# Kernel optimization log

Hardware: AMD Instinct MI355X
Metric: run time of the kernel (lower is better)

Reference implementation:

```python
import jax, jax.numpy as jnp
import numpy as np

N = 50000      # num_nodes
E = 400000     # num_edges
ND = 128       # node_dim (== hidden_dim of GraphNetwork)
HID = 128      # per-head hidden dim in GAT layer
HEADS = 4      # GAT default num_heads
L = 3          # num_layers


def setup_inputs() -> dict:
    key = jax.random.key(0)
    ks = jax.random.split(key, 12)
    s = lambda k, shape, fan: (jax.random.normal(k, shape, jnp.float32) / np.sqrt(fan)).astype(jnp.float32)
    return dict(
        node_features=jax.random.normal(ks[0], (N, ND), jnp.float32),
        edge_index=jax.random.randint(ks[1], (2, E), 0, N, dtype=jnp.int32),
        enc_w1=s(ks[2], (ND, HID), ND), enc_b1=jnp.zeros((HID,), jnp.float32),
        enc_w2=s(ks[3], (HID, HID), HID), enc_b2=jnp.zeros((HID,), jnp.float32),
        gat_W=s(ks[4], (L, HID, HEADS * HID), HID),
        gat_a_src=s(ks[5], (L, HEADS, HID), HID),
        gat_a_dst=s(ks[6], (L, HEADS, HID), HID),
        gat_out_w=s(ks[7], (L, HEADS * HID, HID), HEADS * HID),
        gat_out_b=jnp.zeros((L, HID), jnp.float32),
        out_w1=s(ks[8], (HID, HID), HID), out_b1=jnp.zeros((HID,), jnp.float32),
        out_w2=s(ks[9], (HID, HID), HID), out_b2=jnp.zeros((HID,), jnp.float32),
    )


def _gat_layer(x, row, col, W, a_src, a_dst, ow, ob):
    """One GraphAttentionLayer (eval mode: dropout disabled)."""
    n = x.shape[0]
    h = (x @ W).reshape(n, HEADS, HID)                       # [N,H,D]
    # per-node attention logits (equivalent to (h[row]*a_src).sum(-1) gathered)
    s_src = jnp.einsum('nhd,hd->nh', h, a_src)               # [N,H]
    s_dst = jnp.einsum('nhd,hd->nh', h, a_dst)               # [N,H]
    e = s_src[row] + s_dst[col]                              # [E,H]
    e = jnp.where(e > 0, e, 0.2 * e)                         # LeakyReLU(0.2)
    e_exp = jnp.exp(e)                                       # matches torch: raw exp, no max-shift
    e_sum = jax.ops.segment_sum(e_exp, col, num_segments=n)  # [N,H]
    alpha = e_exp / (e_sum[col] + 1e-8)                      # [E,H]
    msg = h[row] * alpha[:, :, None]                         # [E,H,D]
    out = jax.ops.segment_sum(msg, col, num_segments=n)      # [N,H,D]
    out = out.reshape(n, HEADS * HID) @ ow + ob              # out_proj
    return x + out                                           # residual


def reference(node_features, edge_index, enc_w1, enc_b1, enc_w2, enc_b2,
              gat_W, gat_a_src, gat_a_dst, gat_out_w, gat_out_b,
              out_w1, out_b1, out_w2, out_b2):
    row, col = edge_index[0], edge_index[1]
    # node encoder: Linear-ReLU-Linear
    h = jax.nn.relu(node_features @ enc_w1 + enc_b1) @ enc_w2 + enc_b2
    for i in range(L):
        h = _gat_layer(h, row, col, gat_W[i], gat_a_src[i], gat_a_dst[i],
                       gat_out_w[i], gat_out_b[i])
    # output MLP: Linear-ReLU-Linear
    h = jax.nn.relu(h @ out_w1 + out_b1) @ out_w2 + out_b2
    # batch is None, global_pooling='mean'
    graph_embedding = h.mean(axis=0, keepdims=True)          # [1,HID]
    return h, graph_embedding
```

## Files before the change

kernel.cpp:

```cpp
#include <hip/hip_runtime.h>
#include <math.h>

typedef unsigned short ushort_t;
typedef __attribute__((ext_vector_type(8))) unsigned short ushortx8;
typedef __attribute__((ext_vector_type(4))) unsigned short ushortx4;
typedef __attribute__((ext_vector_type(4))) float floatx4;
typedef __attribute__((ext_vector_type(8))) short frag8;

__device__ __forceinline__ float bf2f(ushort_t u){
  union {unsigned int i; float f;} v; v.i = ((unsigned int)u)<<16; return v.f;
}
__device__ __forceinline__ ushort_t f2bf(float f){
  union {float f; unsigned int i;} v; v.f = f;
  unsigned int x = v.i;
  unsigned int r = x + 0x7fffu + ((x>>16)&1u);
  return (ushort_t)(r>>16);
}

__device__ __forceinline__ void gload16(const void* g, void* l){
  __builtin_amdgcn_global_load_lds(
      (const __attribute__((address_space(1))) unsigned int*)g,
      (__attribute__((address_space(3))) unsigned int*)l, 16, 0, 0);
}

__global__ __launch_bounds__(256) void k_count(const int* __restrict__ col, int* __restrict__ cnt, int E){
  int e = blockIdx.x*256 + threadIdx.x;
  if (e < E) atomicAdd(&cnt[col[e]], 1);
}

__global__ __launch_bounds__(256) void k_scan1(const int* __restrict__ cnt, int* __restrict__ offs,
                                               int* __restrict__ partials, int n){
  __shared__ int buf[256];
  int tid = threadIdx.x;
  int gid = blockIdx.x*256 + tid;
  int v = (gid < n) ? cnt[gid] : 0;
  buf[tid] = v; __syncthreads();
  #pragma unroll
  for (int off=1; off<256; off<<=1){
    int t = (tid >= off) ? buf[tid-off] : 0;
    __syncthreads();
    buf[tid] += t;
    __syncthreads();
  }
  if (gid < n) offs[gid] = buf[tid] - v;
  if (tid == 255) partials[blockIdx.x] = buf[255];
}

__global__ __launch_bounds__(256) void k_scan2(int* __restrict__ partials, int nb){
  __shared__ int buf[256];
  int tid = threadIdx.x;
  int v = (tid < nb) ? partials[tid] : 0;
  buf[tid] = v; __syncthreads();
  #pragma unroll
  for (int off=1; off<256; off<<=1){
    int t = (tid >= off) ? buf[tid-off] : 0;
    __syncthreads();
    buf[tid] += t;
    __syncthreads();
  }
  partials[tid] = buf[tid] - v;
}

__global__ __launch_bounds__(256) void k_scan3(int* __restrict__ offs, const int* __restrict__ partials,
                                               int n, int E){
  int gid = blockIdx.x*256 + threadIdx.x;
  if (gid < n) offs[gid] += partials[blockIdx.x];
  if (blockIdx.x == 0 && threadIdx.x == 0) offs[n] = E;
}

__global__ __launch_bounds__(256) void k_fill(const int* __restrict__ row, const int* __restrict__ col,
                                              const int* __restrict__ offs, int* __restrict__ fill,
                                              int* __restrict__ rowS, int E){
  int e = blockIdx.x*256 + threadIdx.x;
  if (e >= E) return;
  int c = col[e];
  int pos = offs[c] + atomicAdd(&fill[c], 1);
  rowS[pos] = row[e];
}

template<int K, int NC, int CNT>
__global__ __launch_bounds__(256) void k_convT_b(const float* __restrict__ src, ushort_t* __restrict__ dst){
  int idx = blockIdx.x*256 + threadIdx.x;
  if (idx >= CNT*K*NC) return;
  int l = idx / (K*NC);
  int rem = idx - l*(K*NC);
  int k = rem / NC, n = rem - k*NC;
  dst[(size_t)l*K*NC + (size_t)n*K + k] = f2bf(src[idx]);
}

__global__ __launch_bounds__(256) void k_convT4(const float* __restrict__ s0, const float* __restrict__ s1,
                                                const float* __restrict__ s2, const float* __restrict__ s3,
                                                ushort_t* __restrict__ d0, ushort_t* __restrict__ d1,
                                                ushort_t* __restrict__ d2, ushort_t* __restrict__ d3){
  int idx = blockIdx.x*256 + threadIdx.x;
  if (idx >= 4*16384) return;
  int which = idx >> 14;
  int rem = idx & 16383;
  int k = rem >> 7, n = rem & 127;
  const float* s = which==0 ? s0 : which==1 ? s1 : which==2 ? s2 : s3;
  ushort_t*    d = which==0 ? d0 : which==1 ? d1 : which==2 ? d2 : d3;
  d[n*128 + k] = f2bf(s[rem]);
}


__device__ __forceinline__ void la_store(ushort_t* LA, int row, int col, ushort_t v){
  LA[row*128 + ((((col>>3) ^ (row&7))<<3) | (col&7))] = v;
}
__device__ __forceinline__ void la_store8(ushort_t* LA, int row, int cg, ushortx8 v){
  *(ushortx8*)&LA[row*128 + ((cg ^ (row&7))<<3)] = v;
}

__device__ __forceinline__ void stage_tile128_swz(const ushort_t* src, int ld, int row0, int M, int kc,
                                                  ushort_t* lds, int tid){
  #pragma unroll
  for (int i=0;i<8;i++){
    int chunk = tid + 256*i;
    int r = chunk>>4, cg = chunk&15;
    int gr = row0 + r; if (gr >= M) gr = M-1;
    int scg = cg ^ (r&7);
    gload16(src + (size_t)gr*ld + kc + scg*8, (char*)lds + (size_t)chunk*16);
  }
}

template<int NKS>
__device__ __forceinline__ void gemm_swzA_gB(const ushort_t* LA, const ushort_t* __restrict__ BT, int ldb,
                                             floatx4 (&acc)[4][4], int wr,int wc,int lm,int lk){
  #pragma unroll
  for (int ks=0; ks<NKS; ks++){
    frag8 b[4];
    #pragma unroll
    for (int ni=0;ni<4;ni++)
      b[ni] = *(const frag8*)&BT[(size_t)(wc+ni*16+lm)*ldb + ks*32 + lk];
    frag8 a[4];
    int cg = ks*4 + (lk>>3);
    #pragma unroll
    for (int mi=0;mi<4;mi++){
      int row = wr + mi*16 + lm;
      a[mi] = *(const frag8*)&LA[row*128 + ((cg ^ (row&7))<<3)];
    }
    #pragma unroll
    for (int mi=0;mi<4;mi++)
      #pragma unroll
      for (int ni=0;ni<4;ni++)
        acc[mi][ni] = __builtin_amdgcn_mfma_f32_16x16x32_bf16(a[mi], b[ni], acc[mi][ni], 0, 0, 0);
  }
}

__device__ __forceinline__ void zero_acc(floatx4 (&acc)[4][4]){
  #pragma unroll
  for (int i=0;i<4;i++)
    #pragma unroll
    for (int j=0;j<4;j++) acc[i][j] = floatx4{0.f,0.f,0.f,0.f};
}

__device__ __forceinline__ void sdst_block(const floatx4 (&acc)[4][4],
    const float* avec_s, const float* avec_d, float* s_src, float* s_dst, float* sred,
    int head, int bm, int M, int tid, int wid, int lane, int wr, int wc, int lm, int lr4){
  float avs[4], avd[4];
  #pragma unroll
  for (int ni=0;ni<4;ni++){
    int d = wc + ni*16 + lm;
    avs[ni] = avec_s[head*128 + d];
    avd[ni] = avec_d[head*128 + d];
  }
  float pss[4][4], psd[4][4];
  #pragma unroll
  for (int mi=0;mi<4;mi++){
    #pragma unroll
    for (int r=0;r<4;r++){
      float vs = 0.f, vd = 0.f;
      #pragma unroll
      for (int ni=0;ni<4;ni++){
        float v = acc[mi][ni][r];
        vs += v * avs[ni];
        vd += v * avd[ni];
      }
      #pragma unroll
      for (int m=1;m<16;m<<=1){
        vs += __shfl_xor(vs, m);
        vd += __shfl_xor(vd, m);
      }
      pss[mi][r] = vs; psd[mi][r] = vd;
    }
  }
  if (lm == 0){
    #pragma unroll
    for (int mi=0;mi<4;mi++)
      #pragma unroll
      for (int r=0;r<4;r++){
        int rl = wr + mi*16 + lr4 + r;
        sred[0*256 + (wid&1)*128 + rl] = pss[mi][r];
        sred[1*256 + (wid&1)*128 + rl] = psd[mi][r];
      }
  }
  __syncthreads();
  int sd = tid >> 7, rl = tid & 127;
  float v = sred[sd*256 + rl] + sred[sd*256 + 128 + rl];
  int rowg = bm + rl;
  if (rowg < M) (sd ? s_dst : s_src)[(size_t)rowg*4 + head] = v;
}

__device__ __forceinline__ void wgemm_heads(const ushort_t* LA,
    const ushort_t* __restrict__ WT, const float* avs, const float* avd,
    ushort_t* h, float* s_src, float* s_dst, float* sred,
    int bm, int M, int tid, int wid, int lane, int wr, int wc, int lm, int lk, int lr4){
  for (int hb=0; hb<4; hb++){
    __syncthreads();
    floatx4 acc[4][4]; zero_acc(acc);
    gemm_swzA_gB<4>(LA, WT + (size_t)hb*16384, 128, acc, wr, wc, lm, lk);
    #pragma unroll
    for (int mi=0;mi<4;mi++){
      #pragma unroll
      for (int ni=0;ni<4;ni++){
        int colg = wc + ni*16 + lm;
        #pragma unroll
        for (int r=0;r<4;r++){
          int rowg = bm + wr + mi*16 + lr4 + r;
          if (rowg < M) h[(size_t)rowg*512 + hb*128 + colg] = f2bf(acc[mi][ni][r]);
        }
      }
    }
    sdst_block(acc, avs, avd, s_src, s_dst, sred, hb, bm, M, tid, wid, lane, wr, wc, lm, lr4);
  }
}

__global__ __launch_bounds__(256,3) void k_enc(
    const float* __restrict__ nodef,
    const ushort_t* __restrict__ e1T, const float* __restrict__ eb1,
    const ushort_t* __restrict__ e2T, const float* __restrict__ eb2,
    const ushort_t* __restrict__ WT, const float* __restrict__ avs, const float* __restrict__ avd,
    float* __restrict__ x, ushort_t* __restrict__ h,
    float* __restrict__ s_src, float* __restrict__ s_dst, int M)
{
  __shared__ ushort_t LA[128*128];
  __shared__ float sred[512];
  const int tid = threadIdx.x, wid = tid>>6, lane = tid&63;
  const int bm = blockIdx.x*128;
  const int wr = (wid>>1)*64, wc = (wid&1)*64, lm = lane&15, lk = (lane>>4)*8, lr4 = (lane>>4)*4;

  #pragma unroll
  for (int i=0;i<8;i++){
    int chunk = tid + 256*i;
    int r = chunk>>4, cg = chunk&15;
    int gr = bm + r; if (gr >= M) gr = M-1;
    floatx4 lo = *(const floatx4*)(nodef + (size_t)gr*128 + cg*8);
    floatx4 hi = *(const floatx4*)(nodef + (size_t)gr*128 + cg*8 + 4);
    ushortx8 v;
    #pragma unroll
    for (int j=0;j<4;j++){ v[j] = f2bf(lo[j]); v[j+4] = f2bf(hi[j]); }
    la_store8(LA, r, cg, v);
  }
  __syncthreads();

  floatx4 acc[4][4]; zero_acc(acc);
  gemm_swzA_gB<4>(LA, e1T, 128, acc, wr, wc, lm, lk);
  __syncthreads();
  #pragma unroll
  for (int mi=0;mi<4;mi++)
    #pragma unroll
    for (int ni=0;ni<4;ni++){
      int cl = wc + ni*16 + lm;
      float b = eb1[cl];
      #pragma unroll
      for (int r=0;r<4;r++){
        float v = acc[mi][ni][r] + b;
        v = v > 0.f ? v : 0.f;
        la_store(LA, wr + mi*16 + lr4 + r, cl, f2bf(v));
      }
    }
  __syncthreads();

  zero_acc(acc);
  gemm_swzA_gB<4>(LA, e2T, 128, acc, wr, wc, lm, lk);
  __syncthreads();
  #pragma unroll
  for (int mi=0;mi<4;mi++)
    #pragma unroll
    for (int ni=0;ni<4;ni++){
      int cl = wc + ni*16 + lm;
      float b = eb2[cl];
      #pragma unroll
      for (int r=0;r<4;r++){
        int rl = wr + mi*16 + lr4 + r;
        int rowg = bm + rl;
        float v = acc[mi][ni][r] + b;
        if (rowg < M) x[(size_t)rowg*128 + cl] = v;
        la_store(LA, rl, cl, f2bf(v));
      }
    }

  wgemm_heads(LA, WT, avs, avd, h, s_src, s_dst, sred,
              bm, M, tid, wid, lane, wr, wc, lm, lk, lr4);
}

__global__ __launch_bounds__(256,3) void k_mid(
    const ushort_t* __restrict__ msg, const ushort_t* __restrict__ OT, const float* __restrict__ ob,
    const ushort_t* __restrict__ WT, const float* __restrict__ avs, const float* __restrict__ avd,
    float* __restrict__ x, ushort_t* __restrict__ h,
    float* __restrict__ s_src, float* __restrict__ s_dst, int M)
{
  __shared__ ushort_t LA[128*128];
  __shared__ float sred[512];
  const int tid = threadIdx.x, wid = tid>>6, lane = tid&63;
  const int bm = blockIdx.x*128;
  const int wr = (wid>>1)*64, wc = (wid&1)*64, lm = lane&15, lk = (lane>>4)*8, lr4 = (lane>>4)*4;

  floatx4 acc[4][4]; zero_acc(acc);
  for (int kc = 0; kc < 512; kc += 128){
    stage_tile128_swz(msg, 512, bm, M, kc, LA, tid);
    __syncthreads();
    gemm_swzA_gB<4>(LA, OT + kc, 512, acc, wr, wc, lm, lk);
    __syncthreads();
  }
  #pragma unroll
  for (int mi=0;mi<4;mi++)
    #pragma unroll
    for (int ni=0;ni<4;ni++){
      int cl = wc + ni*16 + lm;
      float b = ob[cl];
      #pragma unroll
      for (int r=0;r<4;r++){
        int rl = wr + mi*16 + lr4 + r;
        int rowg = bm + rl;
        float v = acc[mi][ni][r] + b;
        if (rowg < M){
          v += x[(size_t)rowg*128 + cl];
          x[(size_t)rowg*128 + cl] = v;
        }
        la_store(LA, rl, cl, f2bf(v));
      }
    }

  wgemm_heads(LA, WT, avs, avd, h, s_src, s_dst, sred,
              bm, M, tid, wid, lane, wr, wc, lm, lk, lr4);
}

__global__ __launch_bounds__(256,3) void k_tail(
    const ushort_t* __restrict__ msg, const ushort_t* __restrict__ OT, const float* __restrict__ ob,
    const ushort_t* __restrict__ m1T, const float* __restrict__ mb1,
    const ushort_t* __restrict__ m2T, const float* __restrict__ mb2,
    const float* __restrict__ x, float* __restrict__ out, float* __restrict__ cpart, int M)
{
  __shared__ ushort_t LA[128*128];
  __shared__ float sredc[256];
  const int tid = threadIdx.x, wid = tid>>6, lane = tid&63;
  const int bm = blockIdx.x*128;
  const int wr = (wid>>1)*64, wc = (wid&1)*64, lm = lane&15, lk = (lane>>4)*8, lr4 = (lane>>4)*4;

  floatx4 acc[4][4]; zero_acc(acc);
  for (int kc = 0; kc < 512; kc += 128){
    stage_tile128_swz(msg, 512, bm, M, kc, LA, tid);
    __syncthreads();
    gemm_swzA_gB<4>(LA, OT + kc, 512, acc, wr, wc, lm, lk);
    __syncthreads();
  }
  #pragma unroll
  for (int mi=0;mi<4;mi++)
    #pragma unroll
    for (int ni=0;ni<4;ni++){
      int cl = wc + ni*16 + lm;
      float b = ob[cl];
      #pragma unroll
      for (int r=0;r<4;r++){
        int rl = wr + mi*16 + lr4 + r;
        int rowg = bm + rl;
        float v = acc[mi][ni][r] + b;
        if (rowg < M) v += x[(size_t)rowg*128 + cl];
        la_store(LA, rl, cl, f2bf(v));
      }
    }
  __syncthreads();

  zero_acc(acc);
  gemm_swzA_gB<4>(LA, m1T, 128, acc, wr, wc, lm, lk);
  __syncthreads();
  #pragma unroll
  for (int mi=0;mi<4;mi++)
    #pragma unroll
    for (int ni=0;ni<4;ni++){
      int cl = wc + ni*16 + lm;
      float b = mb1[cl];
      #pragma unroll
      for (int r=0;r<4;r++){
        float v = acc[mi][ni][r] + b;
        v = v > 0.f ? v : 0.f;
        la_store(LA, wr + mi*16 + lr4 + r, cl, f2bf(v));
      }
    }
  __syncthreads();

  zero_acc(acc);
  gemm_swzA_gB<4>(LA, m2T, 128, acc, wr, wc, lm, lk);

  float csum[4];
  #pragma unroll
  for (int i=0;i<4;i++) csum[i] = 0.f;
  #pragma unroll
  for (int mi=0;mi<4;mi++)
    #pragma unroll
    for (int ni=0;ni<4;ni++){
      int cl = wc + ni*16 + lm;
      float b = mb2[cl];
      #pragma unroll
      for (int r=0;r<4;r++){
        int rowg = bm + wr + mi*16 + lr4 + r;
        if (rowg < M){
          float v = acc[mi][ni][r] + b;
          out[(size_t)rowg*128 + cl] = v;
          csum[ni] += v;
        }
      }
    }
  __syncthreads();
  #pragma unroll
  for (int ni=0;ni<4;ni++){
    float cs = csum[ni];
    cs += __shfl_xor(cs, 16);
    cs += __shfl_xor(cs, 32);
    if (lane < 16) sredc[(wid>>1)*128 + wc + ni*16 + lane] = cs;
  }
  __syncthreads();
  if (tid < 128) cpart[(size_t)blockIdx.x*128 + tid] = sredc[tid] + sredc[128 + tid];
}

__global__ __launch_bounds__(256) void k_gather(const ushort_t* __restrict__ h,
    const float* __restrict__ s_src, const float* __restrict__ s_dst,
    const int* __restrict__ offs, const int* __restrict__ rowS,
    ushort_t* __restrict__ msg, int N)
{
  int wid = threadIdx.x >> 6, lane = threadIdx.x & 63;
  int n = blockIdx.x*4 + wid;
  if (n >= N) return;
  int beg = offs[n], end = offs[n+1];
  const int sub  = lane & 15;
  const int head = lane >> 4;
  const float sdv = s_dst[(size_t)n*4 + head];
  const int c0 = lane*8;

  float acc[8];
  #pragma unroll
  for (int k=0;k<8;k++) acc[k] = 0.f;
  float dsum = 0.f;

  for (int chunk = beg; chunk < end; chunk += 16){
    int m = end - chunk; if (m > 16) m = 16;
    int q = chunk + (sub < m ? sub : m-1);
    int r_p = rowS[q];
    float ss = s_src[(size_t)r_p*4 + head];
    float e = ss + sdv;
    e = e > 0.f ? e : 0.2f*e;
    float w = __expf(e);
    if (sub >= m) w = 0.f;
    dsum += w;

    int j = 0;
    for (; j+1 < m; j += 2){
      int r0 = __shfl(r_p, j);
      int r1 = __shfl(r_p, j+1);
      float w0 = __shfl(w, head*16 + j);
      float w1 = __shfl(w, head*16 + j+1);
      ushortx8 h0 = *(const ushortx8*)(h + (size_t)r0*512 + c0);
      ushortx8 h1 = *(const ushortx8*)(h + (size_t)r1*512 + c0);
      #pragma unroll
      for (int k=0;k<8;k++) acc[k] += w0 * bf2f(h0[k]);
      #pragma unroll
      for (int k=0;k<8;k++) acc[k] += w1 * bf2f(h1[k]);
    }
    if (j < m){
      int r0 = __shfl(r_p, j);
      float w0 = __shfl(w, head*16 + j);
      ushortx8 h0 = *(const ushortx8*)(h + (size_t)r0*512 + c0);
      #pragma unroll
      for (int k=0;k<8;k++) acc[k] += w0 * bf2f(h0[k]);
    }
  }

  float d = dsum;
  #pragma unroll
  for (int mask=1; mask<16; mask<<=1) d += __shfl_xor(d, mask);
  float invd = 1.0f / (d + 1e-8f);

  ushortx8 o;
  #pragma unroll
  for (int k=0;k<8;k++) o[k] = f2bf(acc[k]*invd);
  __builtin_nontemporal_store(o, (ushortx8*)(msg + (size_t)n*512 + c0));
}

__global__ __launch_bounds__(256) void k_csum2(const float* __restrict__ part, float* __restrict__ out,
                                               int nb, int N){
  __shared__ float buf[256];
  int c = threadIdx.x & 127, half = threadIdx.x >> 7;
  float s = 0.f;
  for (int b = half; b < nb; b += 2) s += part[(size_t)b*128 + c];
  buf[threadIdx.x] = s; __syncthreads();
  if (threadIdx.x < 128) out[c] = (buf[c] + buf[128 + c]) / (float)N;
}

extern "C" void kernel_launch(void* const* d_in, const int* in_sizes, int n_in,
                              void* d_out, int out_size, void* d_ws, size_t ws_size,
                              hipStream_t stream)
{
  const int N = in_sizes[0] / 128;
  const int E = in_sizes[1] / 2;

  const float* nodef  = (const float*)d_in[0];
  const int*   row    = (const int*)d_in[1];
  const int*   col    = row + E;
  const float* enc_w1 = (const float*)d_in[2];
  const float* enc_b1 = (const float*)d_in[3];
  const float* enc_w2 = (const float*)d_in[4];
  const float* enc_b2 = (const float*)d_in[5];
  const float* gat_W  = (const float*)d_in[6];
  const float* a_src  = (const float*)d_in[7];
  const float* a_dst  = (const float*)d_in[8];
  const float* out_w  = (const float*)d_in[9];
  const float* out_b  = (const float*)d_in[10];
  const float* w1     = (const float*)d_in[11];
  const float* b1     = (const float*)d_in[12];
  const float* w2     = (const float*)d_in[13];
  const float* b2     = (const float*)d_in[14];

  char* p = (char*)d_ws;
  auto alloc = [&](size_t bytes)->char*{
    char* r = p; p += (bytes + 255) & ~(size_t)255; return r;
  };
  float*    x     = (float*)   alloc((size_t)N*128*4);
  ushort_t* msg   = (ushort_t*)alloc((size_t)N*512*2);
  ushort_t* h     = (ushort_t*)alloc((size_t)N*512*2);
  float*    s_src = (float*)   alloc((size_t)N*4*4);
  float*    s_dst = (float*)   alloc((size_t)N*4*4);
  int*      offs  = (int*)     alloc(((size_t)N+1)*4);
  int*      rowS  = (int*)     alloc((size_t)E*4);
  int*      cnt   = (int*)     alloc((size_t)N*4);
  int*      fill  = (int*)     alloc((size_t)N*4);
  int*      parts = (int*)     alloc(1024);
  float*    cpart = (float*)   alloc((size_t)((N+127)/128)*128*4);
  ushort_t* wt_e1 = (ushort_t*)alloc(16384*2);
  ushort_t* wt_e2 = (ushort_t*)alloc(16384*2);
  ushort_t* wt_W  = (ushort_t*)alloc((size_t)3*65536*2);
  ushort_t* wt_o  = (ushort_t*)alloc((size_t)3*65536*2);
  ushort_t* wt_m1 = (ushort_t*)alloc(16384*2);
  ushort_t* wt_m2 = (ushort_t*)alloc(16384*2);

  hipMemsetAsync(cnt, 0, (size_t)N*4, stream);
  hipMemsetAsync(fill, 0, (size_t)N*4, stream);

  const int gE = (E + 255)/256;
  const int gN = (N + 255)/256;
  const int gW = (N + 3)/4;
  const int gy = (N + 127)/128;
  dim3 blk(256);

  k_count<<<gE, blk, 0, stream>>>(col, cnt, E);
  k_scan1<<<gN, blk, 0, stream>>>(cnt, offs, parts, N);
  k_scan2<<<1,  blk, 0, stream>>>(parts, gN);
  k_scan3<<<gN, blk, 0, stream>>>(offs, parts, N, E);
  k_fill <<<gE, blk, 0, stream>>>(row, col, offs, fill, rowS, E);

  k_convT4<<<(4*16384+255)/256, blk, 0, stream>>>(enc_w1, enc_w2, w1, w2, wt_e1, wt_e2, wt_m1, wt_m2);
  k_convT_b<128,512,3><<<(3*65536+255)/256, blk, 0, stream>>>(gat_W, wt_W);
  k_convT_b<512,128,3><<<(3*65536+255)/256, blk, 0, stream>>>(out_w, wt_o);

  k_enc<<<gy, blk, 0, stream>>>(nodef, wt_e1, enc_b1, wt_e2, enc_b2,
                                wt_W, a_src, a_dst, x, h, s_src, s_dst, N);

  for (int l = 0; l < 3; l++){
    k_gather<<<gW, blk, 0, stream>>>(h, s_src, s_dst, offs, rowS, msg, N);
    if (l < 2){
      k_mid<<<gy, blk, 0, stream>>>(msg, wt_o + (size_t)l*65536, out_b + (size_t)l*128,
                                    wt_W + (size_t)(l+1)*65536,
                                    a_src + (size_t)(l+1)*512, a_dst + (size_t)(l+1)*512,
                                    x, h, s_src, s_dst, N);
    } else {
      k_tail<<<gy, blk, 0, stream>>>(msg, wt_o + (size_t)2*65536, out_b + (size_t)2*128,
                                     wt_m1, b1, wt_m2, b2,
                                     x, (float*)d_out, cpart, N);
    }
  }
  k_csum2<<<1, blk, 0, stream>>>(cpart, (float*)d_out + (size_t)N*128, gy, N);
}
```

Before: 567.4 us.

## Split head GEMM across grid.y, stage B weights in LDS, ping-pong residual buffers

After: 670.1 us. 1.18x slower.

```diff
diff --git a/kernel.cpp b/kernel.cpp
--- a/kernel.cpp
+++ b/kernel.cpp
@@ -3,7 +3,6 @@
 
 typedef unsigned short ushort_t;
 typedef __attribute__((ext_vector_type(8))) unsigned short ushortx8;
-typedef __attribute__((ext_vector_type(4))) unsigned short ushortx4;
 typedef __attribute__((ext_vector_type(4))) float floatx4;
 typedef __attribute__((ext_vector_type(8))) short frag8;
 
@@ -110,33 +109,35 @@
   *(ushortx8*)&LA[row*128 + ((cg ^ (row&7))<<3)] = v;
 }
 
-__device__ __forceinline__ void stage_tile128_swz(const ushort_t* src, int ld, int row0, int M, int kc,
-                                                  ushort_t* lds, int tid){
-  #pragma unroll
-  for (int i=0;i<8;i++){
+__device__ __forceinline__ void stage64_swz(const ushort_t* __restrict__ src, int ld, int row0, int M,
+                                            int kc, ushort_t* lds, int tid){
+  #pragma unroll
+  for (int i=0;i<4;i++){
     int chunk = tid + 256*i;
-    int r = chunk>>4, cg = chunk&15;
+    int r = chunk>>3, cg = chunk&7;
     int gr = row0 + r; if (gr >= M) gr = M-1;
     int scg = cg ^ (r&7);
     gload16(src + (size_t)gr*ld + kc + scg*8, (char*)lds + (size_t)chunk*16);
   }
 }
 
-template<int NKS>
-__device__ __forceinline__ void gemm_swzA_gB(const ushort_t* LA, const ushort_t* __restrict__ BT, int ldb,
-                                             floatx4 (&acc)[4][4], int wr,int wc,int lm,int lk){
-  #pragma unroll
-  for (int ks=0; ks<NKS; ks++){
-    frag8 b[4];
-    #pragma unroll
-    for (int ni=0;ni<4;ni++)
-      b[ni] = *(const frag8*)&BT[(size_t)(wc+ni*16+lm)*ldb + ks*32 + lk];
-    frag8 a[4];
-    int cg = ks*4 + (lk>>3);
+template<int CWA>
+__device__ __forceinline__ void ldsgemm64(const ushort_t* LA, int kaoff, const ushort_t* LB,
+                                          floatx4 (&acc)[4][4], int wr,int wc,int lm,int lk){
+  #pragma unroll
+  for (int ks=0; ks<2; ks++){
+    frag8 a[4], b[4];
+    int cga = (kaoff + ks*32 + lk) >> 3;
     #pragma unroll
     for (int mi=0;mi<4;mi++){
       int row = wr + mi*16 + lm;
-      a[mi] = *(const frag8*)&LA[row*128 + ((cg ^ (row&7))<<3)];
+      a[mi] = *(const frag8*)&LA[row*(CWA*8) + ((cga ^ (row&7))<<3)];
+    }
+    int cgb = (ks*32 + lk) >> 3;
+    #pragma unroll
+    for (int ni=0;ni<4;ni++){
+      int row = wc + ni*16 + lm;
+      b[ni] = *(const frag8*)&LB[row*64 + ((cgb ^ (row&7))<<3)];
     }
     #pragma unroll
     for (int mi=0;mi<4;mi++)
@@ -153,63 +154,22 @@
     for (int j=0;j<4;j++) acc[i][j] = floatx4{0.f,0.f,0.f,0.f};
 }
 
-__device__ __forceinline__ void sdst_block(const floatx4 (&acc)[4][4],
-    const float* avec_s, const float* avec_d, float* s_src, float* s_dst, float* sred,
-    int head, int bm, int M, int tid, int wid, int lane, int wr, int wc, int lm, int lr4){
-  float avs[4], avd[4];
-  #pragma unroll
-  for (int ni=0;ni<4;ni++){
-    int d = wc + ni*16 + lm;
-    avs[ni] = avec_s[head*128 + d];
-    avd[ni] = avec_d[head*128 + d];
-  }
-  float pss[4][4], psd[4][4];
-  #pragma unroll
-  for (int mi=0;mi<4;mi++){
-    #pragma unroll
-    for (int r=0;r<4;r++){
-      float vs = 0.f, vd = 0.f;
-      #pragma unroll
-      for (int ni=0;ni<4;ni++){
-        float v = acc[mi][ni][r];
-        vs += v * avs[ni];
-        vd += v * avd[ni];
-      }
-      #pragma unroll
-      for (int m=1;m<16;m<<=1){
-        vs += __shfl_xor(vs, m);
-        vd += __shfl_xor(vd, m);
-      }
-      pss[mi][r] = vs; psd[mi][r] = vd;
-    }
-  }
-  if (lm == 0){
+__device__ __forceinline__ void wgemm_2heads(const ushort_t* LA, ushort_t* LB,
+    const ushort_t* __restrict__ WT, const float* __restrict__ avec_s, const float* __restrict__ avec_d,
+    ushort_t* __restrict__ h, float* __restrict__ s_src, float* __restrict__ s_dst, float* sred,
+    int by, int bm, int M, int tid, int wid, int lane, int wr, int wc, int lm, int lk, int lr4){
+  for (int hh=0; hh<2; hh++){
+    int hb = by*2 + hh;
+    floatx4 acc[4][4]; zero_acc(acc);
+    #pragma unroll
+    for (int kph=0; kph<2; kph++){
+      stage64_swz(WT + (size_t)hb*16384, 128, 0, 128, kph*64, LB, tid);
+      __syncthreads();
+      ldsgemm64<16>(LA, kph*64, LB, acc, wr, wc, lm, lk);
+      __syncthreads();
+    }
     #pragma unroll
     for (int mi=0;mi<4;mi++)
-      #pragma unroll
-      for (int r=0;r<4;r++){
-        int rl = wr + mi*16 + lr4 + r;
-        sred[0*256 + (wid&1)*128 + rl] = pss[mi][r];
-        sred[1*256 + (wid&1)*128 + rl] = psd[mi][r];
-      }
-  }
-  __syncthreads();
-  int sd = tid >> 7, rl = tid & 127;
-  float v = sred[sd*256 + rl] + sred[sd*256 + 128 + rl];
-  int rowg = bm + rl;
-  if (rowg < M) (sd ? s_dst : s_src)[(size_t)rowg*4 + head] = v;
-}
-
-__device__ __forceinline__ void wgemm_heads(const ushort_t* LA,
-    const ushort_t* __restrict__ WT, const float* avs, const float* avd,
-    ushort_t* h, float* s_src, float* s_dst, float* sred,
-    int bm, int M, int tid, int wid, int lane, int wr, int wc, int lm, int lk, int lr4){
-  for (int hb=0; hb<4; hb++){
-    __syncthreads();
-    floatx4 acc[4][4]; zero_acc(acc);
-    gemm_swzA_gB<4>(LA, WT + (size_t)hb*16384, 128, acc, wr, wc, lm, lk);
-    #pragma unroll
-    for (int mi=0;mi<4;mi++){
       #pragma unroll
       for (int ni=0;ni<4;ni++){
         int colg = wc + ni*16 + lm;
@@ -219,8 +179,44 @@
           if (rowg < M) h[(size_t)rowg*512 + hb*128 + colg] = f2bf(acc[mi][ni][r]);
         }
       }
-    }
-    sdst_block(acc, avs, avd, s_src, s_dst, sred, hb, bm, M, tid, wid, lane, wr, wc, lm, lr4);
+    float avs[4], avd[4];
+    #pragma unroll
+    for (int ni=0;ni<4;ni++){
+      int d = wc + ni*16 + lm;
+      avs[ni] = avec_s[hb*128 + d];
+      avd[ni] = avec_d[hb*128 + d];
+    }
+    #pragma unroll
+    for (int mi=0;mi<4;mi++){
+      #pragma unroll
+      for (int r=0;r<4;r++){
+        float vs = 0.f, vd = 0.f;
+        #pragma unroll
+        for (int ni=0;ni<4;ni++){
+          float v = acc[mi][ni][r];
+          vs += v * avs[ni];
+          vd += v * avd[ni];
+        }
+        #pragma unroll
+        for (int m=1;m<16;m<<=1){
+          vs += __shfl_xor(vs, m);
+          vd += __shfl_xor(vd, m);
+        }
+        if (lm == 0){
+          int rl = wr + mi*16 + lr4 + r;
+          int half = wid & 1;
+          sred[((hh*2+0)*2 + half)*128 + rl] = vs;
+          sred[((hh*2+1)*2 + half)*128 + rl] = vd;
+        }
+      }
+    }
+  }
+  __syncthreads();
+  for (int q = tid; q < 512; q += 256){
+    int hh = q >> 8, sd = (q >> 7) & 1, rl = q & 127;
+    float v = sred[((hh*2+sd)*2+0)*128 + rl] + sred[((hh*2+sd)*2+1)*128 + rl];
+    int rowg = bm + rl;
+    if (rowg < M) (sd ? s_dst : s_src)[(size_t)rowg*4 + by*2 + hh] = v;
   }
 }
 
@@ -229,13 +225,14 @@
     const ushort_t* __restrict__ e1T, const float* __restrict__ eb1,
     const ushort_t* __restrict__ e2T, const float* __restrict__ eb2,
     const ushort_t* __restrict__ WT, const float* __restrict__ avs, const float* __restrict__ avd,
-    float* __restrict__ x, ushort_t* __restrict__ h,
+    float* __restrict__ xout, ushort_t* __restrict__ h,
     float* __restrict__ s_src, float* __restrict__ s_dst, int M)
 {
   __shared__ ushort_t LA[128*128];
-  __shared__ float sred[512];
+  __shared__ ushort_t LB[128*64];
+  __shared__ float sred[1024];
   const int tid = threadIdx.x, wid = tid>>6, lane = tid&63;
-  const int bm = blockIdx.x*128;
+  const int bm = blockIdx.x*128, by = blockIdx.y;
   const int wr = (wid>>1)*64, wc = (wid&1)*64, lm = lane&15, lk = (lane>>4)*8, lr4 = (lane>>4)*4;
 
   #pragma unroll
@@ -253,8 +250,13 @@
   __syncthreads();
 
   floatx4 acc[4][4]; zero_acc(acc);
-  gemm_swzA_gB<4>(LA, e1T, 128, acc, wr, wc, lm, lk);
-  __syncthreads();
+  #pragma unroll
+  for (int kph=0; kph<2; kph++){
+    stage64_swz(e1T, 128, 0, 128, kph*64, LB, tid);
+    __syncthreads();
+    ldsgemm64<16>(LA, kph*64, LB, acc, wr, wc, lm, lk);
+    __syncthreads();
+  }
   #pragma unroll
   for (int mi=0;mi<4;mi++)
     #pragma unroll
@@ -268,11 +270,14 @@
         la_store(LA, wr + mi*16 + lr4 + r, cl, f2bf(v));
       }
     }
-  __syncthreads();
-
   zero_acc(acc);
-  gemm_swzA_gB<4>(LA, e2T, 128, acc, wr, wc, lm, lk);
-  __syncthreads();
+  #pragma unroll
+  for (int kph=0; kph<2; kph++){
+    stage64_swz(e2T, 128, 0, 128, kph*64, LB, tid);
+    __syncthreads();
+    ldsgemm64<16>(LA, kph*64, LB, acc, wr, wc, lm, lk);
+    __syncthreads();
+  }
   #pragma unroll
   for (int mi=0;mi<4;mi++)
     #pragma unroll
@@ -284,32 +289,34 @@
         int rl = wr + mi*16 + lr4 + r;
         int rowg = bm + rl;
         float v = acc[mi][ni][r] + b;
-        if (rowg < M) x[(size_t)rowg*128 + cl] = v;
+        if (by == 0 && rowg < M) xout[(size_t)rowg*128 + cl] = v;
         la_store(LA, rl, cl, f2bf(v));
       }
     }
 
-  wgemm_heads(LA, WT, avs, avd, h, s_src, s_dst, sred,
-              bm, M, tid, wid, lane, wr, wc, lm, lk, lr4);
+  wgemm_2heads(LA, LB, WT, avs, avd, h, s_src, s_dst, sred,
+               by, bm, M, tid, wid, lane, wr, wc, lm, lk, lr4);
 }
 
 __global__ __launch_bounds__(256,3) void k_mid(
     const ushort_t* __restrict__ msg, const ushort_t* __restrict__ OT, const float* __restrict__ ob,
     const ushort_t* __restrict__ WT, const float* __restrict__ avs, const float* __restrict__ avd,
-    float* __restrict__ x, ushort_t* __restrict__ h,
+    const float* __restrict__ xin, float* __restrict__ xout, ushort_t* __restrict__ h,
     float* __restrict__ s_src, float* __restrict__ s_dst, int M)
 {
   __shared__ ushort_t LA[128*128];
-  __shared__ float sred[512];
+  __shared__ ushort_t LB[128*64];
+  __shared__ float sred[1024];
   const int tid = threadIdx.x, wid = tid>>6, lane = tid&63;
-  const int bm = blockIdx.x*128;
+  const int bm = blockIdx.x*128, by = blockIdx.y;
   const int wr = (wid>>1)*64, wc = (wid&1)*64, lm = lane&15, lk = (lane>>4)*8, lr4 = (lane>>4)*4;
 
   floatx4 acc[4][4]; zero_acc(acc);
-  for (int kc = 0; kc < 512; kc += 128){
-    stage_tile128_swz(msg, 512, bm, M, kc, LA, tid);
-    __syncthreads();
-    gemm_swzA_gB<4>(LA, OT + kc, 512, acc, wr, wc, lm, lk);
+  for (int kc = 0; kc < 512; kc += 64){
+    stage64_swz(msg, 512, bm, M, kc, LA, tid);
+    stage64_swz(OT,  512, 0, 128, kc, LB, tid);
+    __syncthreads();
+    ldsgemm64<8>(LA, 0, LB, acc, wr, wc, lm, lk);
     __syncthreads();
   }
   #pragma unroll
@@ -324,34 +331,36 @@
         int rowg = bm + rl;
         float v = acc[mi][ni][r] + b;
         if (rowg < M){
-          v += x[(size_t)rowg*128 + cl];
-          x[(size_t)rowg*128 + cl] = v;
+          v += xin[(size_t)rowg*128 + cl];
+          if (by == 0) xout[(size_t)rowg*128 + cl] = v;
         }
         la_store(LA, rl, cl, f2bf(v));
       }
     }
 
-  wgemm_heads(LA, WT, avs, avd, h, s_src, s_dst, sred,
-              bm, M, tid, wid, lane, wr, wc, lm, lk, lr4);
+  wgemm_2heads(LA, LB, WT, avs, avd, h, s_src, s_dst, sred,
+               by, bm, M, tid, wid, lane, wr, wc, lm, lk, lr4);
 }
 
 __global__ __launch_bounds__(256,3) void k_tail(
     const ushort_t* __restrict__ msg, const ushort_t* __restrict__ OT, const float* __restrict__ ob,
     const ushort_t* __restrict__ m1T, const float* __restrict__ mb1,
     const ushort_t* __restrict__ m2T, const float* __restrict__ mb2,
-    const float* __restrict__ x, float* __restrict__ out, float* __restrict__ cpart, int M)
+    const float* __restrict__ xin, float* __restrict__ out, float* __restrict__ cpart, int M)
 {
   __shared__ ushort_t LA[128*128];
-  __shared__ float sredc[256];
+  __shared__ ushort_t LB[128*64];
+  __shared__ float sred[1024];
   const int tid = threadIdx.x, wid = tid>>6, lane = tid&63;
   const int bm = blockIdx.x*128;
   const int wr = (wid>>1)*64, wc = (wid&1)*64, lm = lane&15, lk = (lane>>4)*8, lr4 = (lane>>4)*4;
 
   floatx4 acc[4][4]; zero_acc(acc);
-  for (int kc = 0; kc < 512; kc += 128){
-    stage_tile128_swz(msg, 512, bm, M, kc, LA, tid);
-    __syncthreads();
-    gemm_swzA_gB<4>(LA, OT + kc, 512, acc, wr, wc, lm, lk);
+  for (int kc = 0; kc < 512; kc += 64){
+    stage64_swz(msg, 512, bm, M, kc, LA, tid);
+    stage64_swz(OT,  512, 0, 128, kc, LB, tid);
+    __syncthreads();
+    ldsgemm64<8>(LA, 0, LB, acc, wr, wc, lm, lk);
     __syncthreads();
   }
   #pragma unroll
@@ -365,15 +374,18 @@
         int rl = wr + mi*16 + lr4 + r;
         int rowg = bm + rl;
         float v = acc[mi][ni][r] + b;
-        if (rowg < M) v += x[(size_t)rowg*128 + cl];
+        if (rowg < M) v += xin[(size_t)rowg*128 + cl];
         la_store(LA, rl, cl, f2bf(v));
       }
     }
-  __syncthreads();
-
   zero_acc(acc);
-  gemm_swzA_gB<4>(LA, m1T, 128, acc, wr, wc, lm, lk);
-  __syncthreads();
+  #pragma unroll
+  for (int kph=0; kph<2; kph++){
+    stage64_swz(m1T, 128, 0, 128, kph*64, LB, tid);
+    __syncthreads();
+    ldsgemm64<16>(LA, kph*64, LB, acc, wr, wc, lm, lk);
+    __syncthreads();
+  }
   #pragma unroll
   for (int mi=0;mi<4;mi++)
     #pragma unroll
@@ -387,11 +399,14 @@
         la_store(LA, wr + mi*16 + lr4 + r, cl, f2bf(v));
       }
     }
-  __syncthreads();
-
   zero_acc(acc);
-  gemm_swzA_gB<4>(LA, m2T, 128, acc, wr, wc, lm, lk);
-
+  #pragma unroll
+  for (int kph=0; kph<2; kph++){
+    stage64_swz(m2T, 128, 0, 128, kph*64, LB, tid);
+    __syncthreads();
+    ldsgemm64<16>(LA, kph*64, LB, acc, wr, wc, lm, lk);
+    __syncthreads();
+  }
   float csum[4];
   #pragma unroll
   for (int i=0;i<4;i++) csum[i] = 0.f;
@@ -411,16 +426,15 @@
         }
       }
     }
-  __syncthreads();
   #pragma unroll
   for (int ni=0;ni<4;ni++){
     float cs = csum[ni];
     cs += __shfl_xor(cs, 16);
     cs += __shfl_xor(cs, 32);
-    if (lane < 16) sredc[(wid>>1)*128 + wc + ni*16 + lane] = cs;
+    if (lane < 16) sred[(wid>>1)*128 + wc + ni*16 + lane] = cs;
   }
   __syncthreads();
-  if (tid < 128) cpart[(size_t)blockIdx.x*128 + tid] = sredc[tid] + sredc[128 + tid];
+  if (tid < 128) cpart[(size_t)blockIdx.x*128 + tid] = sred[tid] + sred[128 + tid];
 }
 
 __global__ __launch_bounds__(256) void k_gather(const ushort_t* __restrict__ h,
@@ -524,7 +538,8 @@
   auto alloc = [&](size_t bytes)->char*{
     char* r = p; p += (bytes + 255) & ~(size_t)255; return r;
   };
-  float*    x     = (float*)   alloc((size_t)N*128*4);
+  float*    xA    = (float*)   alloc((size_t)N*128*4);
+  float*    xB    = (float*)   alloc((size_t)N*128*4);
   ushort_t* msg   = (ushort_t*)alloc((size_t)N*512*2);
   ushort_t* h     = (ushort_t*)alloc((size_t)N*512*2);
   float*    s_src = (float*)   alloc((size_t)N*4*4);
@@ -561,21 +576,21 @@
   k_convT_b<128,512,3><<<(3*65536+255)/256, blk, 0, stream>>>(gat_W, wt_W);
   k_convT_b<512,128,3><<<(3*65536+255)/256, blk, 0, stream>>>(out_w, wt_o);
 
-  k_enc<<<gy, blk, 0, stream>>>(nodef, wt_e1, enc_b1, wt_e2, enc_b2,
-                                wt_W, a_src, a_dst, x, h, s_src, s_dst, N);
-
-  for (int l = 0; l < 3; l++){
-    k_gather<<<gW, blk, 0, stream>>>(h, s_src, s_dst, offs, rowS, msg, N);
-    if (l < 2){
-      k_mid<<<gy, blk, 0, stream>>>(msg, wt_o + (size_t)l*65536, out_b + (size_t)l*128,
-                                    wt_W + (size_t)(l+1)*65536,
-                                    a_src + (size_t)(l+1)*512, a_dst + (size_t)(l+1)*512,
-                                    x, h, s_src, s_dst, N);
-    } else {
-      k_tail<<<gy, blk, 0, stream>>>(msg, wt_o + (size_t)2*65536, out_b + (size_t)2*128,
-                                     wt_m1, b1, wt_m2, b2,
-                                     x, (float*)d_out, cpart, N);
-    }
-  }
+  k_enc<<<dim3(gy,2), blk, 0, stream>>>(nodef, wt_e1, enc_b1, wt_e2, enc_b2,
+                                        wt_W, a_src, a_dst, xA, h, s_src, s_dst, N);
+
+  k_gather<<<gW, blk, 0, stream>>>(h, s_src, s_dst, offs, rowS, msg, N);
+  k_mid<<<dim3(gy,2), blk, 0, stream>>>(msg, wt_o, out_b,
+                                        wt_W + (size_t)1*65536, a_src + 512, a_dst + 512,
+                                        xA, xB, h, s_src, s_dst, N);
+  k_gather<<<gW, blk, 0, stream>>>(h, s_src, s_dst, offs, rowS, msg, N);
+  k_mid<<<dim3(gy,2), blk, 0, stream>>>(msg, wt_o + (size_t)1*65536, out_b + 128,
+                                        wt_W + (size_t)2*65536, a_src + 1024, a_dst + 1024,
+                                        xB, xA, h, s_src, s_dst, N);
+  k_gather<<<gW, blk, 0, stream>>>(h, s_src, s_dst, offs, rowS, msg, N);
+  k_tail<<<gy, blk, 0, stream>>>(msg, wt_o + (size_t)2*65536, out_b + 256,
+                                 wt_m1, b1, wt_m2, b2,
+                                 xA, (float*)d_out, cpart, N);
+
   k_csum2<<<1, blk, 0, stream>>>(cpart, (float*)d_out + (size_t)N*128, gy, N);
 }
```
